# Performance work log

Hardware: AMD Instinct MI355X
Metric: run time of the kernel (lower is better)

The kernel has to match this reference:

```python
import jax, jax.numpy as jnp
import numpy as np

D_MODEL = 256
NHEAD = 4
HEAD_DIM = D_MODEL // NHEAD
TEMP = float(np.sqrt(D_MODEL / NHEAD))
EPS = 1e-5


def layernorm(x, g, b):
    mu = jnp.mean(x, axis=-1, keepdims=True)
    var = jnp.mean(jnp.square(x - mu), axis=-1, keepdims=True)
    return (x - mu) * jax.lax.rsqrt(var + EPS) * g + b


def setup_inputs() -> dict:
    key = jax.random.key(0)
    ks = jax.random.split(key, 8)
    B, S, D = 4, 4096, D_MODEL
    s = 1.0 / np.sqrt(D)
    return {
        "x": jax.random.normal(ks[0], (B, S, D), dtype=jnp.float32),
        "Wq": jax.random.normal(ks[1], (D, D), dtype=jnp.float32) * s,
        "Wk": jax.random.normal(ks[2], (D, D), dtype=jnp.float32) * s,
        "Wv": jax.random.normal(ks[3], (D, D), dtype=jnp.float32) * s,
        "g1": jnp.ones((D,), jnp.float32),
        "b1": jnp.zeros((D,), jnp.float32),
        "g2": jnp.ones((D,), jnp.float32),
        "b2": jnp.zeros((D,), jnp.float32),
        "W1": jax.random.normal(ks[4], (D, D), dtype=jnp.float32) * s,
        "bf1": jnp.zeros((D,), jnp.float32),
        "W2": jax.random.normal(ks[5], (D, D), dtype=jnp.float32) * s,
        "bf2": jnp.zeros((D,), jnp.float32),
    }


def reference(x, Wq, Wk, Wv, g1, b1, g2, b2, W1, bf1, W2, bf2):
    B, S, D = x.shape
    xn = layernorm(x, g1, b1)
    # torch Linear (no bias): y = x @ W.T
    q = (xn @ Wq.T).reshape(B, S, NHEAD, HEAD_DIM)
    k = (xn @ Wk.T).reshape(B, S, NHEAD, HEAD_DIM)
    v = (xn @ Wv.T).reshape(B, S, NHEAD, HEAD_DIM)
    scores = jnp.einsum("bqhd,bkhd->bhqk", q, k) / TEMP
    causal = jnp.tril(jnp.ones((S, S), dtype=bool))  # True = keep
    scores = jnp.where(causal, scores, -jnp.inf)
    attn = jax.nn.softmax(scores, axis=-1)
    att = jnp.einsum("bhqk,bkhd->bqhd", attn, v).reshape(B, S, D)
    xt = x + att
    h = layernorm(xt, g2, b2)
    ffn = jax.nn.relu(h @ W1.T + bf1) @ W2.T + bf2
    return xt + ffn
```

## Files before the change

### kernel.cpp

```cpp
#include <hip/hip_runtime.h>
#include <math.h>

#define D_MODEL 256
#define NHEAD 4
#define HEAD_DIM 64
#define SEQ 4096
#define BATCH 4
#define MROWS (BATCH * SEQ)

typedef __attribute__((ext_vector_type(8))) short short8;
typedef __attribute__((ext_vector_type(4))) short short4v;
typedef __attribute__((ext_vector_type(8))) __bf16 bf16x8;
typedef __attribute__((ext_vector_type(4))) float f32x4;

__device__ inline short f2bf(float f) {
  unsigned u = __float_as_uint(f);
  u += 0x7fffu + ((u >> 16) & 1u);
  return (short)(u >> 16);
}
__device__ inline bf16x8 as_bf8(short8 s) {
  union { short8 s; bf16x8 b; } u;
  u.s = s;
  return u.b;
}
__device__ __forceinline__ void g2lds16(const void* g, void* l) {
  __builtin_amdgcn_global_load_lds(
      (const __attribute__((address_space(1))) unsigned int*)g,
      (__attribute__((address_space(3))) unsigned int*)l, 16, 0, 0);
}

__device__ __forceinline__ f32x4 mfma16bf(short4v a, short4v b, f32x4 c) {
#if __has_builtin(__builtin_amdgcn_mfma_f32_16x16x16bf16_1k)
  return __builtin_amdgcn_mfma_f32_16x16x16bf16_1k(a, b, c, 0, 0, 0);
#else
  asm("v_mfma_f32_16x16x16_bf16 %0, %1, %2, %0" : "+v"(c) : "v"(a), "v"(b));
  return c;
#endif
}

#define QSCALE 0.1803368801111204f

__global__ __launch_bounds__(256) void wcvt(const float* __restrict__ s0, const float* __restrict__ s1,
                                            const float* __restrict__ s2, const float* __restrict__ s3,
                                            const float* __restrict__ s4, short* __restrict__ d0,
                                            short* __restrict__ d1, short* __restrict__ d2,
                                            short* __restrict__ d3, short* __restrict__ d4) {
  int mat = blockIdx.x >> 5;
  int e = ((blockIdx.x & 31) * 256 + threadIdx.x) * 8;
  const float* s = mat == 0 ? s0 : mat == 1 ? s1 : mat == 2 ? s2 : mat == 3 ? s3 : s4;
  short* d = mat == 0 ? d0 : mat == 1 ? d1 : mat == 2 ? d2 : mat == 3 ? d3 : d4;
  int n = e >> 8, k0 = e & 255;
  float4 f0 = *(const float4*)(s + n * 256 + k0);
  float4 f1 = *(const float4*)(s + n * 256 + k0 + 4);
  short8 o = {f2bf(f0.x), f2bf(f0.y), f2bf(f0.z), f2bf(f0.w),
              f2bf(f1.x), f2bf(f1.y), f2bf(f1.z), f2bf(f1.w)};
  int chunk = k0 >> 5, g = (k0 >> 3) & 3;
  *(short8*)(d + n * 256 + chunk * 32 + ((g ^ (n & 3)) * 8)) = o;
}

__global__ __launch_bounds__(256) void qkv_ln(
    const short* __restrict__ Wqi, const short* __restrict__ Wki,
    const short* __restrict__ Wvi, const float* __restrict__ x,
    const float* __restrict__ g1v, const float* __restrict__ b1v,
    short* __restrict__ qo, short* __restrict__ kimg, short* __restrict__ vimg) {
  __shared__ __align__(16) short Xs[64 * 256];
  const int t = threadIdx.x, lane = t & 63, w = t >> 6;
  const int l15 = lane & 15, quad = lane >> 4;
  const int m0 = blockIdx.x * 64;
  const int which = blockIdx.y;
  const short* Wb = which == 0 ? Wqi : which == 1 ? Wki : Wvi;

  {
    const int r = t >> 5, c8 = t & 31;
    float4 ga = *(const float4*)(g1v + c8 * 8);
    float4 gc = *(const float4*)(g1v + c8 * 8 + 4);
    float4 ba = *(const float4*)(b1v + c8 * 8);
    float4 bc = *(const float4*)(b1v + c8 * 8 + 4);
#pragma unroll
    for (int pass = 0; pass < 8; pass++) {
      int row = pass * 8 + r;
      const float* xr = x + (size_t)(m0 + row) * D_MODEL + c8 * 8;
      float4 a = *(const float4*)xr;
      float4 c = *(const float4*)(xr + 4);
      float s = a.x + a.y + a.z + a.w + c.x + c.y + c.z + c.w;
#pragma unroll
      for (int off = 16; off > 0; off >>= 1) s += __shfl_xor(s, off);
      float mu = s * (1.0f / D_MODEL);
      float d0 = a.x - mu, d1 = a.y - mu, d2 = a.z - mu, d3 = a.w - mu;
      float d4 = c.x - mu, d5 = c.y - mu, d6 = c.z - mu, d7 = c.w - mu;
      float ss = d0 * d0 + d1 * d1 + d2 * d2 + d3 * d3 + d4 * d4 + d5 * d5 + d6 * d6 + d7 * d7;
#pragma unroll
      for (int off = 16; off > 0; off >>= 1) ss += __shfl_xor(ss, off);
      float rstd = rsqrtf(ss * (1.0f / D_MODEL) + 1e-5f);
      short8 ov = {f2bf(d0 * rstd * ga.x + ba.x), f2bf(d1 * rstd * ga.y + ba.y),
                   f2bf(d2 * rstd * ga.z + ba.z), f2bf(d3 * rstd * ga.w + ba.w),
                   f2bf(d4 * rstd * gc.x + bc.x), f2bf(d5 * rstd * gc.y + bc.y),
                   f2bf(d6 * rstd * gc.z + bc.z), f2bf(d7 * rstd * gc.w + bc.w)};
      int chunk = c8 >> 2, gr = c8 & 3;
      *(short8*)&Xs[row * 256 + chunk * 32 + ((gr ^ (row & 3)) * 8)] = ov;
    }
  }
  __syncthreads();

  const short* xb = &Xs[l15 * 256 + ((quad ^ (l15 & 3)) * 8)];
  const short* wb = Wb + (size_t)(w * 64 + l15) * 256 + ((quad ^ (l15 & 3)) * 8);

  f32x4 acc[4][4];
#pragma unroll
  for (int i = 0; i < 4; i++)
#pragma unroll
    for (int j = 0; j < 4; j++) acc[i][j] = (f32x4){0.f, 0.f, 0.f, 0.f};

#pragma unroll
  for (int kf = 0; kf < 8; kf++) {
    bf16x8 fx[4], fw[4];
#pragma unroll
    for (int i = 0; i < 4; i++) {
      fx[i] = as_bf8(*(const short8*)(xb + i * 4096 + kf * 32));
      fw[i] = as_bf8(*(const short8*)(wb + i * 4096 + kf * 32));
    }
    if (which == 2) {
#pragma unroll
      for (int mt = 0; mt < 4; mt++)
#pragma unroll
        for (int nt = 0; nt < 4; nt++)
          acc[mt][nt] = __builtin_amdgcn_mfma_f32_16x16x32_bf16(fx[mt], fw[nt], acc[mt][nt], 0, 0, 0);
    } else {
#pragma unroll
      for (int mt = 0; mt < 4; mt++)
#pragma unroll
        for (int nt = 0; nt < 4; nt++)
          acc[mt][nt] = __builtin_amdgcn_mfma_f32_16x16x32_bf16(fw[nt], fx[mt], acc[mt][nt], 0, 0, 0);
    }
  }

#pragma unroll
  for (int mt = 0; mt < 4; mt++)
#pragma unroll
    for (int nt = 0; nt < 4; nt++) {
      f32x4 v = acc[mt][nt];
      if (which == 2) {
        int n = w * 64 + nt * 16 + l15;
        int mr = m0 + mt * 16 + quad * 4;
        int b = mr >> 12, s = mr & 4095, h = n >> 6, d = n & 63;
        size_t off = ((size_t)(b * NHEAD + h) * 64 + (s >> 6)) * 4096 +
                     (size_t)d * 64 + ((((s & 63) >> 3) ^ (d & 7)) * 8) + (s & 7);
        short4v o = {f2bf(v[0]), f2bf(v[1]), f2bf(v[2]), f2bf(v[3])};
        *(short4v*)(vimg + off) = o;
      } else {
        int m = m0 + mt * 16 + l15;
        int nb = w * 64 + nt * 16 + quad * 4;
        if (which == 0) {
          v *= QSCALE;
          short4v o = {f2bf(v[0]), f2bf(v[1]), f2bf(v[2]), f2bf(v[3])};
          *(short4v*)(qo + (size_t)m * D_MODEL + nb) = o;
        } else {
          int b = m >> 12, s = m & 4095, h = nb >> 6, d = nb & 63;
          size_t off = ((size_t)(b * NHEAD + h) * 64 + (s >> 6)) * 4096 +
                       (size_t)(s & 63) * 64 + (((d >> 3) ^ (s & 7)) * 8) + (d & 7);
          short4v o = {f2bf(v[0]), f2bf(v[1]), f2bf(v[2]), f2bf(v[3])};
          *(short4v*)(kimg + off) = o;
        }
      }
    }
}

__global__ __launch_bounds__(256) void ffn_ln(
    const short* __restrict__ w1i, const short* __restrict__ w2i,
    const float* __restrict__ g2v, const float* __restrict__ b2v,
    const float* __restrict__ bf1, const float* __restrict__ bf2,
    const float* __restrict__ xt, float* __restrict__ out) {
  __shared__ __align__(16) short Hs[32 * 256];
  __shared__ __align__(16) short F1s[32 * 264];
  const int t = threadIdx.x, lane = t & 63, w = t >> 6;
  const int l15 = lane & 15, quad = lane >> 4;
  const int m0 = blockIdx.x * 32;

  {
    const int r = t >> 5, c8 = t & 31;
    float4 ga = *(const float4*)(g2v + c8 * 8);
    float4 gc = *(const float4*)(g2v + c8 * 8 + 4);
    float4 ba = *(const float4*)(b2v + c8 * 8);
    float4 bc = *(const float4*)(b2v + c8 * 8 + 4);
#pragma unroll
    for (int pass = 0; pass < 4; pass++) {
      int row = pass * 8 + r;
      const float* xr = xt + (size_t)(m0 + row) * D_MODEL + c8 * 8;
      float4 a = *(const float4*)xr;
      float4 c = *(const float4*)(xr + 4);
      float s = a.x + a.y + a.z + a.w + c.x + c.y + c.z + c.w;
#pragma unroll
      for (int off = 16; off > 0; off >>= 1) s += __shfl_xor(s, off);
      float mu = s * (1.0f / D_MODEL);
      float d0 = a.x - mu, d1 = a.y - mu, d2 = a.z - mu, d3 = a.w - mu;
      float d4 = c.x - mu, d5 = c.y - mu, d6 = c.z - mu, d7 = c.w - mu;
      float ss = d0 * d0 + d1 * d1 + d2 * d2 + d3 * d3 + d4 * d4 + d5 * d5 + d6 * d6 + d7 * d7;
#pragma unroll
      for (int off = 16; off > 0; off >>= 1) ss += __shfl_xor(ss, off);
      float rstd = rsqrtf(ss * (1.0f / D_MODEL) + 1e-5f);
      short8 ov = {f2bf(d0 * rstd * ga.x + ba.x), f2bf(d1 * rstd * ga.y + ba.y),
                   f2bf(d2 * rstd * ga.z + ba.z), f2bf(d3 * rstd * ga.w + ba.w),
                   f2bf(d4 * rstd * gc.x + bc.x), f2bf(d5 * rstd * gc.y + bc.y),
                   f2bf(d6 * rstd * gc.z + bc.z), f2bf(d7 * rstd * gc.w + bc.w)};
      int chunk = c8 >> 2, gr = c8 & 3;
      *(short8*)&Hs[row * 256 + chunk * 32 + ((gr ^ (row & 3)) * 8)] = ov;
    }
  }
  __syncthreads();

  const short* hb = &Hs[l15 * 256 + ((quad ^ (l15 & 3)) * 8)];
  const short* w1b = w1i + (size_t)(w * 64 + l15) * 256 + ((quad ^ (l15 & 3)) * 8);
  const short* w2b = w2i + (size_t)(w * 64 + l15) * 256 + ((quad ^ (l15 & 3)) * 8);

  f32x4 a1[2][4];
#pragma unroll
  for (int i = 0; i < 2; i++)
#pragma unroll
    for (int j = 0; j < 4; j++) a1[i][j] = (f32x4){0.f, 0.f, 0.f, 0.f};
#pragma unroll
  for (int kf = 0; kf < 8; kf++) {
    bf16x8 fh[2], fw1[4];
#pragma unroll
    for (int i = 0; i < 2; i++) fh[i] = as_bf8(*(const short8*)(hb + i * 4096 + kf * 32));
#pragma unroll
    for (int i = 0; i < 4; i++) fw1[i] = as_bf8(*(const short8*)(w1b + i * 4096 + kf * 32));
#pragma unroll
    for (int mt = 0; mt < 2; mt++)
#pragma unroll
      for (int nt = 0; nt < 4; nt++)
        a1[mt][nt] = __builtin_amdgcn_mfma_f32_16x16x32_bf16(fw1[nt], fh[mt], a1[mt][nt], 0, 0, 0);
  }
#pragma unroll
  for (int mt = 0; mt < 2; mt++)
#pragma unroll
    for (int nt = 0; nt < 4; nt++) {
      int n1 = w * 64 + nt * 16 + quad * 4;
      int ml = mt * 16 + l15;
      float4 bv = *(const float4*)(bf1 + n1);
      f32x4 v = a1[mt][nt];
      short4v o = {f2bf(fmaxf(v[0] + bv.x, 0.f)), f2bf(fmaxf(v[1] + bv.y, 0.f)),
                   f2bf(fmaxf(v[2] + bv.z, 0.f)), f2bf(fmaxf(v[3] + bv.w, 0.f))};
      *(short4v*)&F1s[ml * 264 + n1] = o;
    }
  __syncthreads();

  const short* fb = &F1s[l15 * 264 + quad * 8];
  f32x4 a2[2][4];
#pragma unroll
  for (int i = 0; i < 2; i++)
#pragma unroll
    for (int j = 0; j < 4; j++) a2[i][j] = (f32x4){0.f, 0.f, 0.f, 0.f};
#pragma unroll
  for (int kf = 0; kf < 8; kf++) {
    bf16x8 ff[2], fw2[4];
#pragma unroll
    for (int i = 0; i < 2; i++) ff[i] = as_bf8(*(const short8*)(fb + i * 16 * 264 + kf * 32));
#pragma unroll
    for (int i = 0; i < 4; i++) fw2[i] = as_bf8(*(const short8*)(w2b + i * 4096 + kf * 32));
#pragma unroll
    for (int mt = 0; mt < 2; mt++)
#pragma unroll
      for (int nt = 0; nt < 4; nt++)
        a2[mt][nt] = __builtin_amdgcn_mfma_f32_16x16x32_bf16(ff[mt], fw2[nt], a2[mt][nt], 0, 0, 0);
  }
#pragma unroll
  for (int mt = 0; mt < 2; mt++)
#pragma unroll
    for (int nt = 0; nt < 4; nt++) {
      int n2 = w * 64 + nt * 16 + l15;
      int mg = m0 + mt * 16 + quad * 4;
      float bv = bf2[n2];
      f32x4 v = a2[mt][nt];
#pragma unroll
      for (int r = 0; r < 4; r++) {
        size_t a = (size_t)(mg + r) * D_MODEL + n2;
        out[a] = v[r] + bv + xt[a];
      }
    }
}

__global__ __launch_bounds__(256, 3) void attn_v7(const short* __restrict__ qb,
                                                  const short* __restrict__ kimg,
                                                  const short* __restrict__ vimg,
                                                  const float* __restrict__ x,
                                                  float* __restrict__ xt) {
  __shared__ __align__(16) short Ks[2 * 4096];
  __shared__ __align__(16) short Vs[2 * 4096];

  const int t = threadIdx.x, lane = t & 63, w = t >> 6;
  const int quad = lane >> 4, l15 = lane & 15, l7 = lane & 7;
  const int qa = quad & 1, q1 = quad >> 1;
  const int yy = blockIdx.y, gq = yy >> 4, rq = yy & 15;
  const int qt = gq == 0 ? 63 - rq : gq == 1 ? rq : gq == 2 ? 47 - rq : 16 + rq;
  const int bh = blockIdx.x, b = bh >> 2, h = bh & 3;
  const int ldsoff = __builtin_amdgcn_readfirstlane(w * 512);
  const short* kb_bh = kimg + (size_t)bh * 64 * 4096;
  const short* vb_bh = vimg + (size_t)bh * 64 * 4096;

  const int sb = w * 32;
  const int q0 = qt * 64;

  const short* ka[2][2];
#pragma unroll
  for (int kk = 0; kk < 2; kk++)
#pragma unroll
    for (int dh = 0; dh < 2; dh++)
      ka[kk][dh] = &Ks[(sb + kk * 16 + l15) * 64 + (((quad + 4 * dh) ^ l7) * 8)];
  const short* va[2];
#pragma unroll
  for (int kk = 0; kk < 2; kk++) {
    int sk = sb + kk * 16;
    va[kk] = &Vs[(sk >> 6) * 4096 + l15 * 64 + ((((((sk & 63) >> 3) | q1) ^ l7)) * 8) + qa * 4];
  }

  bf16x8 qf[4][2];
  {
    const short* qpb = qb + ((size_t)(b * SEQ + q0 + l15)) * D_MODEL + h * HEAD_DIM + quad * 8;
#pragma unroll
    for (int qq = 0; qq < 4; qq++) {
      qf[qq][0] = as_bf8(*(const short8*)(qpb + qq * 16 * D_MODEL));
      qf[qq][1] = as_bf8(*(const short8*)(qpb + qq * 16 * D_MODEL + 32));
    }
  }

  f32x4 oacc[4][4];
#pragma unroll
  for (int i = 0; i < 4; i++)
#pragma unroll
    for (int j = 0; j < 4; j++) oacc[i][j] = (f32x4){0.f, 0.f, 0.f, 0.f};
  float lrun[4] = {0.f, 0.f, 0.f, 0.f};

  const int niter = (qt + 2) >> 1;

#pragma unroll
  for (int i = 0; i < 4; i++) {
    g2lds16(kb_bh + i * 2048 + t * 8, &Ks[i * 2048 + ldsoff]);
    g2lds16(vb_bh + i * 2048 + t * 8, &Vs[i * 2048 + ldsoff]);
  }
  __syncthreads();

  for (int it = 0; it < niter; it++) {
    const int j0 = it * 128;
    const bool active = (j0 + sb) <= (q0 + 63);

    uint2 pu[2][4];
    if (active) {
      f32x4 st[2][4];
#pragma unroll
      for (int kk = 0; kk < 2; kk++) {
        bf16x8 k0 = as_bf8(*(const short8*)(ka[kk][0]));
        bf16x8 k1 = as_bf8(*(const short8*)(ka[kk][1]));
#pragma unroll
        for (int qq = 0; qq < 4; qq++) {
          f32x4 z = (f32x4){0.f, 0.f, 0.f, 0.f};
          z = __builtin_amdgcn_mfma_f32_16x16x32_bf16(k0, qf[qq][0], z, 0, 0, 0);
          z = __builtin_amdgcn_mfma_f32_16x16x32_bf16(k1, qf[qq][1], z, 0, 0, 0);
          st[kk][qq] = z;
        }
      }
      if (j0 + sb + 31 > q0) {
#pragma unroll
        for (int kk = 0; kk < 2; kk++) {
          int kbase = j0 + sb + kk * 16 + quad * 4;
#pragma unroll
          for (int qq = 0; qq < 4; qq++) {
            int qrow = q0 + qq * 16 + l15;
#pragma unroll
            for (int r = 0; r < 4; r++)
              if (kbase + r > qrow) st[kk][qq][r] = -1e30f;
          }
        }
      }
#pragma unroll
      for (int kk = 0; kk < 2; kk++)
#pragma unroll
        for (int qq = 0; qq < 4; qq++) {
          float p0 = __builtin_amdgcn_exp2f(st[kk][qq][0]);
          float p1 = __builtin_amdgcn_exp2f(st[kk][qq][1]);
          float p2 = __builtin_amdgcn_exp2f(st[kk][qq][2]);
          float p3 = __builtin_amdgcn_exp2f(st[kk][qq][3]);
          lrun[qq] += p0 + p1 + p2 + p3;
          pu[kk][qq].x = (__float_as_uint(p0) >> 16) | (__float_as_uint(p1) & 0xffff0000u);
          pu[kk][qq].y = (__float_as_uint(p2) >> 16) | (__float_as_uint(p3) & 0xffff0000u);
        }
    }

    __syncthreads();

    if (it + 1 < niter) {
      const short* kc_base = kb_bh + (size_t)(2 * (it + 1)) * 4096;
#pragma unroll
      for (int i = 0; i < 4; i++)
        g2lds16(kc_base + i * 2048 + t * 8, &Ks[i * 2048 + ldsoff]);
    }

    if (active) {
#pragma unroll
      for (int kk = 0; kk < 2; kk++) {
        union { uint2 u; short4v s; } pb0, pb1, pb2, pb3;
        pb0.u = pu[kk][0];
        pb1.u = pu[kk][1];
        pb2.u = pu[kk][2];
        pb3.u = pu[kk][3];
#pragma unroll
        for (int dt = 0; dt < 4; dt++) {
          short4v vv = *(const short4v*)(va[kk] + dt * 1024);
          oacc[dt][0] = mfma16bf(vv, pb0.s, oacc[dt][0]);
          oacc[dt][1] = mfma16bf(vv, pb1.s, oacc[dt][1]);
          oacc[dt][2] = mfma16bf(vv, pb2.s, oacc[dt][2]);
          oacc[dt][3] = mfma16bf(vv, pb3.s, oacc[dt][3]);
        }
      }
    }

    __syncthreads();

    if (it + 1 < niter) {
      const short* vc_base = vb_bh + (size_t)(2 * (it + 1)) * 4096;
#pragma unroll
      for (int i = 0; i < 4; i++)
        g2lds16(vc_base + i * 2048 + t * 8, &Vs[i * 2048 + ldsoff]);
    }
  }

#pragma unroll
  for (int qq = 0; qq < 4; qq++) {
    lrun[qq] += __shfl_xor(lrun[qq], 16);
    lrun[qq] += __shfl_xor(lrun[qq], 32);
  }
  float* ored = (float*)Ks;
  float* lred = (float*)Vs;
  __syncthreads();
  if (quad == 0) {
#pragma unroll
    for (int qq = 0; qq < 4; qq++) lred[(w * 4 + qq) * 16 + l15] = lrun[qq];
  }
#pragma unroll
  for (int rr = 1; rr < 4; rr++) {
#pragma unroll
    for (int dt = 0; dt < 4; dt++)
      if (dt == ((w + rr) & 3)) {
#pragma unroll
        for (int qq = 0; qq < 4; qq++)
#pragma unroll
          for (int e = 0; e < 4; e++)
            ored[dt * 1024 + (quad * 4 + e) * 64 + qq * 16 + l15] = oacc[dt][qq][e];
      }
    __syncthreads();
#pragma unroll
    for (int dt = 0; dt < 4; dt++)
      if (dt == w) {
#pragma unroll
        for (int qq = 0; qq < 4; qq++)
#pragma unroll
          for (int e = 0; e < 4; e++)
            oacc[dt][qq][e] += ored[dt * 1024 + (quad * 4 + e) * 64 + qq * 16 + l15];
      }
    if (rr < 3) __syncthreads();
  }
  float inv[4];
#pragma unroll
  for (int qq = 0; qq < 4; qq++) {
    float s = lred[qq * 16 + l15] + lred[(4 + qq) * 16 + l15] +
              lred[(8 + qq) * 16 + l15] + lred[(12 + qq) * 16 + l15];
    inv[qq] = 1.0f / s;
  }
#pragma unroll
  for (int dt = 0; dt < 4; dt++)
    if (dt == w) {
      size_t rowb = ((size_t)(b * SEQ + q0 + l15)) * D_MODEL + h * HEAD_DIM + dt * 16 + quad * 4;
#pragma unroll
      for (int qq = 0; qq < 4; qq++) {
        size_t a = rowb + (size_t)qq * 16 * D_MODEL;
        float4 xv = *(const float4*)(x + a);
        float4 o = make_float4(oacc[dt][qq][0] * inv[qq] + xv.x,
                               oacc[dt][qq][1] * inv[qq] + xv.y,
                               oacc[dt][qq][2] * inv[qq] + xv.z,
                               oacc[dt][qq][3] * inv[qq] + xv.w);
        *(float4*)(xt + a) = o;
      }
    }
}

extern "C" void kernel_launch(void* const* d_in, const int* in_sizes, int n_in,
                              void* d_out, int out_size, void* d_ws,
                              size_t ws_size, hipStream_t stream) {
  const float* x = (const float*)d_in[0];
  const float* Wq = (const float*)d_in[1];
  const float* Wk = (const float*)d_in[2];
  const float* Wv = (const float*)d_in[3];
  const float* g1 = (const float*)d_in[4];
  const float* b1 = (const float*)d_in[5];
  const float* g2 = (const float*)d_in[6];
  const float* b2 = (const float*)d_in[7];
  const float* W1 = (const float*)d_in[8];
  const float* bf1 = (const float*)d_in[9];
  const float* W2 = (const float*)d_in[10];
  const float* bf2 = (const float*)d_in[11];
  float* out = (float*)d_out;

  char* ws = (char*)d_ws;
  float* xt = (float*)ws;
  short* q_bf = (short*)(ws + (16u << 20));
  short* kimg = (short*)(ws + (24u << 20));
  short* vimg = (short*)(ws + (32u << 20));
  short* wq_i = (short*)(ws + (48u << 20));
  short* wk_i = wq_i + 65536;
  short* wv_i = wq_i + 2 * 65536;
  short* w1_i = wq_i + 3 * 65536;
  short* w2_i = wq_i + 4 * 65536;

  dim3 blk(256);
  wcvt<<<160, blk, 0, stream>>>(Wq, Wk, Wv, W1, W2, wq_i, wk_i, wv_i, w1_i, w2_i);
  qkv_ln<<<dim3(MROWS / 64, 3), blk, 0, stream>>>(wq_i, wk_i, wv_i, x, g1, b1,
                                                  q_bf, kimg, vimg);
  attn_v7<<<dim3(16, 64), blk, 0, stream>>>(q_bf, kimg, vimg, x, xt);
  ffn_ln<<<MROWS / 32, blk, 0, stream>>>(w1_i, w2_i, g2, b2, bf1, bf2, xt, out);
}
```

Baseline: 171.0 us.

## Double-buffer K in LDS and stream V directly into registers

The attention kernel now double-buffers K tiles in LDS, so the next tile's async copy overlaps the current QK^T step and one of the two barriers per iteration goes away. V is no longer staged through LDS. Each wave loads its V fragments straight from global memory into ping-pong register arrays one iteration ahead, with the loop unrolled by two to swap buffers. The cost is more registers (16 short4 per buffer pair) and uncoalesced direct global V loads, which can reduce occupancy or add memory latency.

New measurement: 273.8 us. +60.1%, slower.

```diff
diff --git a/kernel.cpp b/kernel.cpp
--- a/kernel.cpp
+++ b/kernel.cpp
@@ -279,13 +279,13 @@
     }
 }
 
-__global__ __launch_bounds__(256, 3) void attn_v7(const short* __restrict__ qb,
-                                                  const short* __restrict__ kimg,
-                                                  const short* __restrict__ vimg,
-                                                  const float* __restrict__ x,
-                                                  float* __restrict__ xt) {
-  __shared__ __align__(16) short Ks[2 * 4096];
-  __shared__ __align__(16) short Vs[2 * 4096];
+__global__ __launch_bounds__(256, 3) void attn_v13(const short* __restrict__ qb,
+                                                   const short* __restrict__ kimg,
+                                                   const short* __restrict__ vimg,
+                                                   const float* __restrict__ x,
+                                                   float* __restrict__ xt) {
+  __shared__ __align__(16) short Ks[2 * 8192];
+  __shared__ float lred[256];
 
   const int t = threadIdx.x, lane = t & 63, w = t >> 6;
   const int quad = lane >> 4, l15 = lane & 15, l7 = lane & 7;
@@ -300,17 +300,17 @@
   const int sb = w * 32;
   const int q0 = qt * 64;
 
-  const short* ka[2][2];
+  int ka_off[2][2];
 #pragma unroll
   for (int kk = 0; kk < 2; kk++)
 #pragma unroll
     for (int dh = 0; dh < 2; dh++)
-      ka[kk][dh] = &Ks[(sb + kk * 16 + l15) * 64 + (((quad + 4 * dh) ^ l7) * 8)];
-  const short* va[2];
+      ka_off[kk][dh] = (sb + kk * 16 + l15) * 64 + (((quad + 4 * dh) ^ l7) * 8);
+  int voff[2];
 #pragma unroll
   for (int kk = 0; kk < 2; kk++) {
     int sk = sb + kk * 16;
-    va[kk] = &Vs[(sk >> 6) * 4096 + l15 * 64 + ((((((sk & 63) >> 3) | q1) ^ l7)) * 8) + qa * 4];
+    voff[kk] = (sk >> 6) * 4096 + l15 * 64 + ((((sk & 63) >> 3) | q1) ^ l7) * 8 + qa * 4;
   }
 
   bf16x8 qf[4][2];
@@ -332,24 +332,34 @@
 
   const int niter = (qt + 2) >> 1;
 
-#pragma unroll
-  for (int i = 0; i < 4; i++) {
+  short4v vA[2][4], vB[2][4];
+
+#pragma unroll
+  for (int i = 0; i < 4; i++)
     g2lds16(kb_bh + i * 2048 + t * 8, &Ks[i * 2048 + ldsoff]);
-    g2lds16(vb_bh + i * 2048 + t * 8, &Vs[i * 2048 + ldsoff]);
+  if (sb <= q0 + 63) {
+#pragma unroll
+    for (int kk = 0; kk < 2; kk++)
+#pragma unroll
+      for (int dt = 0; dt < 4; dt++)
+        vA[kk][dt] = *(const short4v*)(vb_bh + voff[kk] + dt * 1024);
   }
   __syncthreads();
 
-  for (int it = 0; it < niter; it++) {
+  auto body = [&](short4v(&VC)[2][4], short4v(&VN)[2][4], int it) {
     const int j0 = it * 128;
     const bool active = (j0 + sb) <= (q0 + 63);
+    const bool knext = (it + 1 < niter);
+    const bool vnext = knext && ((j0 + 128 + sb) <= (q0 + 63));
+    const short* kb = &Ks[(it & 1) * 8192];
 
     uint2 pu[2][4];
+    f32x4 st[2][4];
     if (active) {
-      f32x4 st[2][4];
 #pragma unroll
       for (int kk = 0; kk < 2; kk++) {
-        bf16x8 k0 = as_bf8(*(const short8*)(ka[kk][0]));
-        bf16x8 k1 = as_bf8(*(const short8*)(ka[kk][1]));
+        bf16x8 k0 = as_bf8(*(const short8*)(kb + ka_off[kk][0]));
+        bf16x8 k1 = as_bf8(*(const short8*)(kb + ka_off[kk][1]));
 #pragma unroll
         for (int qq = 0; qq < 4; qq++) {
           f32x4 z = (f32x4){0.f, 0.f, 0.f, 0.f};
@@ -358,6 +368,23 @@
           st[kk][qq] = z;
         }
       }
+    }
+    if (knext) {
+      const short* kc = kb_bh + (size_t)(it + 1) * 8192;
+      short* kd = &Ks[((it + 1) & 1) * 8192];
+#pragma unroll
+      for (int i = 0; i < 4; i++)
+        g2lds16(kc + i * 2048 + t * 8, kd + i * 2048 + ldsoff);
+    }
+    if (vnext) {
+      const short* vc = vb_bh + (size_t)(it + 1) * 8192;
+#pragma unroll
+      for (int kk = 0; kk < 2; kk++)
+#pragma unroll
+        for (int dt = 0; dt < 4; dt++)
+          VN[kk][dt] = *(const short4v*)(vc + voff[kk] + dt * 1024);
+    }
+    if (active) {
       if (j0 + sb + 31 > q0) {
 #pragma unroll
         for (int kk = 0; kk < 2; kk++) {
@@ -383,18 +410,6 @@
           pu[kk][qq].x = (__float_as_uint(p0) >> 16) | (__float_as_uint(p1) & 0xffff0000u);
           pu[kk][qq].y = (__float_as_uint(p2) >> 16) | (__float_as_uint(p3) & 0xffff0000u);
         }
-    }
-
-    __syncthreads();
-
-    if (it + 1 < niter) {
-      const short* kc_base = kb_bh + (size_t)(2 * (it + 1)) * 4096;
-#pragma unroll
-      for (int i = 0; i < 4; i++)
-        g2lds16(kc_base + i * 2048 + t * 8, &Ks[i * 2048 + ldsoff]);
-    }
-
-    if (active) {
 #pragma unroll
       for (int kk = 0; kk < 2; kk++) {
         union { uint2 u; short4v s; } pb0, pb1, pb2, pb3;
@@ -404,7 +419,7 @@
         pb3.u = pu[kk][3];
 #pragma unroll
         for (int dt = 0; dt < 4; dt++) {
-          short4v vv = *(const short4v*)(va[kk] + dt * 1024);
+          short4v vv = VC[kk][dt];
           oacc[dt][0] = mfma16bf(vv, pb0.s, oacc[dt][0]);
           oacc[dt][1] = mfma16bf(vv, pb1.s, oacc[dt][1]);
           oacc[dt][2] = mfma16bf(vv, pb2.s, oacc[dt][2]);
@@ -412,15 +427,15 @@
         }
       }
     }
-
     __syncthreads();
-
-    if (it + 1 < niter) {
-      const short* vc_base = vb_bh + (size_t)(2 * (it + 1)) * 4096;
-#pragma unroll
-      for (int i = 0; i < 4; i++)
-        g2lds16(vc_base + i * 2048 + t * 8, &Vs[i * 2048 + ldsoff]);
-    }
+  };
+
+  int it = 0;
+  while (it < niter) {
+    body(vA, vB, it);
+    if (++it >= niter) break;
+    body(vB, vA, it);
+    ++it;
   }
 
 #pragma unroll
@@ -429,7 +444,6 @@
     lrun[qq] += __shfl_xor(lrun[qq], 32);
   }
   float* ored = (float*)Ks;
-  float* lred = (float*)Vs;
   __syncthreads();
   if (quad == 0) {
 #pragma unroll
@@ -514,6 +528,6 @@
   wcvt<<<160, blk, 0, stream>>>(Wq, Wk, Wv, W1, W2, wq_i, wk_i, wv_i, w1_i, w2_i);
   qkv_ln<<<dim3(MROWS / 64, 3), blk, 0, stream>>>(wq_i, wk_i, wv_i, x, g1, b1,
                                                   q_bf, kimg, vimg);
-  attn_v7<<<dim3(16, 64), blk, 0, stream>>>(q_bf, kimg, vimg, x, xt);
+  attn_v13<<<dim3(16, 64), blk, 0, stream>>>(q_bf, kimg, vimg, x, xt);
   ffn_ln<<<MROWS / 32, blk, 0, stream>>>(w1_i, w2_i, g2, b2, bf1, bf2, xt, out);
 }
```

## Double-buffer K/V tiles in LDS to overlap prefetch with attention compute

Applied to the files above, without the earlier changes.

The attention kernel now keeps two LDS buffers each for K and V and issues the next tile's global-to-LDS loads at the top of each iteration, before computing on the current buffer. This removes one of the two barriers per iteration and the serialization between loading and consuming tiles. The cost is twice the LDS footprint per block, which may lower the number of resident blocks per CU.

Result: slower. 200.3 us (+17.1%).

```diff
diff --git a/kernel.cpp b/kernel.cpp
--- a/kernel.cpp
+++ b/kernel.cpp
@@ -279,13 +279,13 @@
     }
 }
 
-__global__ __launch_bounds__(256, 3) void attn_v7(const short* __restrict__ qb,
-                                                  const short* __restrict__ kimg,
-                                                  const short* __restrict__ vimg,
-                                                  const float* __restrict__ x,
-                                                  float* __restrict__ xt) {
-  __shared__ __align__(16) short Ks[2 * 4096];
-  __shared__ __align__(16) short Vs[2 * 4096];
+__global__ __launch_bounds__(256, 3) void attn_v14(const short* __restrict__ qb,
+                                                   const short* __restrict__ kimg,
+                                                   const short* __restrict__ vimg,
+                                                   const float* __restrict__ x,
+                                                   float* __restrict__ xt) {
+  __shared__ __align__(16) short Ks[2 * 8192];
+  __shared__ __align__(16) short Vs[2 * 8192];
 
   const int t = threadIdx.x, lane = t & 63, w = t >> 6;
   const int quad = lane >> 4, l15 = lane & 15, l7 = lane & 7;
@@ -300,17 +300,17 @@
   const int sb = w * 32;
   const int q0 = qt * 64;
 
-  const short* ka[2][2];
+  int ka_off[2][2];
 #pragma unroll
   for (int kk = 0; kk < 2; kk++)
 #pragma unroll
     for (int dh = 0; dh < 2; dh++)
-      ka[kk][dh] = &Ks[(sb + kk * 16 + l15) * 64 + (((quad + 4 * dh) ^ l7) * 8)];
-  const short* va[2];
+      ka_off[kk][dh] = (sb + kk * 16 + l15) * 64 + (((quad + 4 * dh) ^ l7) * 8);
+  int va_off[2];
 #pragma unroll
   for (int kk = 0; kk < 2; kk++) {
     int sk = sb + kk * 16;
-    va[kk] = &Vs[(sk >> 6) * 4096 + l15 * 64 + ((((((sk & 63) >> 3) | q1) ^ l7)) * 8) + qa * 4];
+    va_off[kk] = (sk >> 6) * 4096 + l15 * 64 + ((((sk & 63) >> 3) | q1) ^ l7) * 8 + qa * 4;
   }
 
   bf16x8 qf[4][2];
@@ -343,13 +343,26 @@
     const int j0 = it * 128;
     const bool active = (j0 + sb) <= (q0 + 63);
 
-    uint2 pu[2][4];
+    if (it + 1 < niter) {
+      const short* kc = kb_bh + (size_t)(it + 1) * 8192;
+      const short* vc = vb_bh + (size_t)(it + 1) * 8192;
+      short* kd = &Ks[((it + 1) & 1) * 8192];
+      short* vd = &Vs[((it + 1) & 1) * 8192];
+#pragma unroll
+      for (int i = 0; i < 4; i++) {
+        g2lds16(kc + i * 2048 + t * 8, kd + i * 2048 + ldsoff);
+        g2lds16(vc + i * 2048 + t * 8, vd + i * 2048 + ldsoff);
+      }
+    }
+
     if (active) {
+      const short* kbuf = &Ks[(it & 1) * 8192];
+      const short* vbuf = &Vs[(it & 1) * 8192];
       f32x4 st[2][4];
 #pragma unroll
       for (int kk = 0; kk < 2; kk++) {
-        bf16x8 k0 = as_bf8(*(const short8*)(ka[kk][0]));
-        bf16x8 k1 = as_bf8(*(const short8*)(ka[kk][1]));
+        bf16x8 k0 = as_bf8(*(const short8*)(kbuf + ka_off[kk][0]));
+        bf16x8 k1 = as_bf8(*(const short8*)(kbuf + ka_off[kk][1]));
 #pragma unroll
         for (int qq = 0; qq < 4; qq++) {
           f32x4 z = (f32x4){0.f, 0.f, 0.f, 0.f};
@@ -371,6 +384,7 @@
           }
         }
       }
+      uint2 pu[2][4];
 #pragma unroll
       for (int kk = 0; kk < 2; kk++)
 #pragma unroll
@@ -383,18 +397,6 @@
           pu[kk][qq].x = (__float_as_uint(p0) >> 16) | (__float_as_uint(p1) & 0xffff0000u);
           pu[kk][qq].y = (__float_as_uint(p2) >> 16) | (__float_as_uint(p3) & 0xffff0000u);
         }
-    }
-
-    __syncthreads();
-
-    if (it + 1 < niter) {
-      const short* kc_base = kb_bh + (size_t)(2 * (it + 1)) * 4096;
-#pragma unroll
-      for (int i = 0; i < 4; i++)
-        g2lds16(kc_base + i * 2048 + t * 8, &Ks[i * 2048 + ldsoff]);
-    }
-
-    if (active) {
 #pragma unroll
       for (int kk = 0; kk < 2; kk++) {
         union { uint2 u; short4v s; } pb0, pb1, pb2, pb3;
@@ -404,7 +406,7 @@
         pb3.u = pu[kk][3];
 #pragma unroll
         for (int dt = 0; dt < 4; dt++) {
-          short4v vv = *(const short4v*)(va[kk] + dt * 1024);
+          short4v vv = *(const short4v*)(vbuf + va_off[kk] + dt * 1024);
           oacc[dt][0] = mfma16bf(vv, pb0.s, oacc[dt][0]);
           oacc[dt][1] = mfma16bf(vv, pb1.s, oacc[dt][1]);
           oacc[dt][2] = mfma16bf(vv, pb2.s, oacc[dt][2]);
@@ -414,13 +416,6 @@
     }
 
     __syncthreads();
-
-    if (it + 1 < niter) {
-      const short* vc_base = vb_bh + (size_t)(2 * (it + 1)) * 4096;
-#pragma unroll
-      for (int i = 0; i < 4; i++)
-        g2lds16(vc_base + i * 2048 + t * 8, &Vs[i * 2048 + ldsoff]);
-    }
   }
 
 #pragma unroll
@@ -514,6 +509,6 @@
   wcvt<<<160, blk, 0, stream>>>(Wq, Wk, Wv, W1, W2, wq_i, wk_i, wv_i, w1_i, w2_i);
   qkv_ln<<<dim3(MROWS / 64, 3), blk, 0, stream>>>(wq_i, wk_i, wv_i, x, g1, b1,
                                                   q_bf, kimg, vimg);
-  attn_v7<<<dim3(16, 64), blk, 0, stream>>>(q_bf, kimg, vimg, x, xt);
+  attn_v14<<<dim3(16, 64), blk, 0, stream>>>(q_bf, kimg, vimg, x, xt);
   ffn_ln<<<MROWS / 32, blk, 0, stream>>>(w1_i, w2_i, g2, b2, bf1, bf2, xt, out);
 }
```
